# Performance work log

Hardware: AMD Instinct MI355X
Metric: run time of the kernel (lower is better)

Reference implementation:

```python
import jax, jax.numpy as jnp
import numpy as np


def setup_inputs() -> dict:
    key = jax.random.key(0)
    ks = jax.random.split(key, 5)
    B, S, D, F = 4, 2048, 1024, 4096
    scale_w1 = 1.0 / np.sqrt(D)
    scale_w2 = 1.0 / np.sqrt(F)
    return {
        "hidden_states": jax.random.normal(ks[0], (B, S, D), dtype=jnp.float32),
        "W1": jax.random.normal(ks[1], (F, D), dtype=jnp.float32) * scale_w1,
        "b1": jax.random.normal(ks[2], (F,), dtype=jnp.float32) * 0.02,
        "W2": jax.random.normal(ks[3], (D, F), dtype=jnp.float32) * scale_w2,
        "b2": jax.random.normal(ks[4], (D,), dtype=jnp.float32) * 0.02,
    }


def _sigmoid_poly(h):
    # cubic polynomial sigmoid approximation: 0.5 + 0.25*h - 0.0208*h^3
    h2 = h * h
    h3 = h2 * h
    return 0.5 + 0.25 * h + (-0.0208) * h3


def reference(hidden_states, W1, b1, W2, b2):
    # secure linear projection == plain affine: x @ W.T + b
    h = jnp.einsum("bsd,fd->bsf", hidden_states, W1) + b1  # [B,S,F]
    sw = h * _sigmoid_poly(h)                               # swish via poly sigmoid
    out = jnp.einsum("bsf,df->bsd", sw, W2) + b2            # [B,S,D]
    return out
```

## Files before the change

### kernel.cpp

```cpp
#include <hip/hip_runtime.h>
#include <hip/hip_bf16.h>

typedef __bf16 bf16_t;
typedef __bf16 bf16x8 __attribute__((ext_vector_type(8)));
typedef float f32x4 __attribute__((ext_vector_type(4)));

__global__ __launch_bounds__(256) void cast3_f32_to_bf16(
    const float* __restrict__ a, bf16_t* __restrict__ ao, int na8,
    const float* __restrict__ b, bf16_t* __restrict__ bo, int nb8,
    const float* __restrict__ c, bf16_t* __restrict__ co, int nc8) {
  int i = blockIdx.x * blockDim.x + threadIdx.x;
  const float* in;
  bf16_t* out;
  int j;
  if (i < na8) {
    in = a; out = ao; j = i;
  } else if (i < na8 + nb8) {
    in = b; out = bo; j = i - na8;
  } else if (i < na8 + nb8 + nc8) {
    in = c; out = co; j = i - na8 - nb8;
  } else {
    return;
  }
  const float4* in4 = (const float4*)in;
  float4 f0 = in4[2 * j];
  float4 f1 = in4[2 * j + 1];
  bf16x8 o;
  o[0] = (bf16_t)f0.x; o[1] = (bf16_t)f0.y;
  o[2] = (bf16_t)f0.z; o[3] = (bf16_t)f0.w;
  o[4] = (bf16_t)f1.x; o[5] = (bf16_t)f1.y;
  o[6] = (bf16_t)f1.z; o[7] = (bf16_t)f1.w;
  ((bf16x8*)out)[j] = o;
}

__device__ __forceinline__ void gload_lds16(const bf16_t* g, bf16_t* l) {
  __builtin_amdgcn_global_load_lds(
      (const __attribute__((address_space(1))) void*)g,
      (__attribute__((address_space(3))) void*)l,
      16, 0, 0);
}

template <bool SWISH>
__global__ __launch_bounds__(256) void gemm_bt(
    const bf16_t* __restrict__ A, const bf16_t* __restrict__ B,
    const float* __restrict__ bias, void* __restrict__ Cout,
    int M, int N, int K, int XW, int px, int py) {
  const int tid  = threadIdx.x;
  const int wave = tid >> 6;
  const int lane = tid & 63;

  const int bid = blockIdx.x;
  const int xcd = bid & 7;
  const int idx = bid >> 3;
  const int cx = xcd % XW;
  const int cy = xcd / XW;
  const int bx = cx * px + idx % px;
  const int by = cy * py + idx / px;
  const int tileM = by << 7;
  const int tileN = bx << 7;

  __shared__ __align__(16) bf16_t sA[128 * 64];
  __shared__ __align__(16) bf16_t sB[128 * 64];

  const int srow = (wave << 3) + (lane >> 3);
  const int gcol = (((lane & 7) ^ (lane >> 3)) << 3);
  const bf16_t* gA = A + (size_t)(tileM + srow) * K + gcol;
  const bf16_t* gB = B + (size_t)(tileN + srow) * K + gcol;
  bf16_t* lA = sA + (size_t)(wave << 3) * 64;
  bf16_t* lB = sB + (size_t)(wave << 3) * 64;

  const int wr = wave >> 1;
  const int wc = wave & 1;
  const int fRow = lane & 15;
  const int c0 = lane >> 4;
  const int swz = lane & 7;
  const int p0 = c0 ^ swz;
  const int d1 = (((p0 ^ 4) - p0) << 3);
  const bf16x8* pA[4];
  const bf16x8* pB[4];
#pragma unroll
  for (int i = 0; i < 4; ++i) {
    const int lrA = wr * 64 + i * 16 + fRow;
    const int lrB = wc * 64 + i * 16 + fRow;
    pA[i] = (const bf16x8*)(sA + lrA * 64 + p0 * 8);
    pB[i] = (const bf16x8*)(sB + lrB * 64 + p0 * 8);
  }

  f32x4 acc[4][4] = {};

  for (int kt = 0; kt < K; kt += 64) {
#pragma unroll
    for (int r = 0; r < 4; ++r) {
      gload_lds16(gA + kt + (size_t)(r * 32) * K, lA + r * 32 * 64);
      gload_lds16(gB + kt + (size_t)(r * 32) * K, lB + r * 32 * 64);
    }
    __syncthreads();

    bf16x8 a0[4], b0[4];
#pragma unroll
    for (int i = 0; i < 4; ++i) {
      a0[i] = *pA[i];
      b0[i] = *pB[i];
    }
#pragma unroll
    for (int i = 0; i < 4; ++i)
#pragma unroll
      for (int j = 0; j < 4; ++j)
        acc[i][j] = __builtin_amdgcn_mfma_f32_16x16x32_bf16(
            a0[i], b0[j], acc[i][j], 0, 0, 0);

    bf16x8 a1[4], b1[4];
#pragma unroll
    for (int i = 0; i < 4; ++i) {
      a1[i] = *(const bf16x8*)((const bf16_t*)pA[i] + d1);
      b1[i] = *(const bf16x8*)((const bf16_t*)pB[i] + d1);
    }
#pragma unroll
    for (int i = 0; i < 4; ++i)
#pragma unroll
      for (int j = 0; j < 4; ++j)
        acc[i][j] = __builtin_amdgcn_mfma_f32_16x16x32_bf16(
            a1[i], b1[j], acc[i][j], 0, 0, 0);
    __syncthreads();
  }

  const int cRow0 = tileM + wr * 64 + ((lane >> 4) << 2);
  const int cCol0 = tileN + wc * 64 + (lane & 15);
#pragma unroll
  for (int j = 0; j < 4; ++j) {
    const int col = cCol0 + j * 16;
    const float bv = bias[col];
#pragma unroll
    for (int i = 0; i < 4; ++i) {
      const int row = cRow0 + i * 16;
#pragma unroll
      for (int r = 0; r < 4; ++r) {
        float h = acc[i][j][r] + bv;
        if constexpr (SWISH) {
          float h3 = h * h * h;
          float sw = h * (0.5f + 0.25f * h - 0.0208f * h3);
          ((bf16_t*)Cout)[(size_t)(row + r) * N + col] = (bf16_t)sw;
        } else {
          ((float*)Cout)[(size_t)(row + r) * N + col] = h;
        }
      }
    }
  }
}

extern "C" void kernel_launch(void* const* d_in, const int* in_sizes, int n_in,
                              void* d_out, int out_size, void* d_ws,
                              size_t ws_size, hipStream_t stream) {
  const float* X  = (const float*)d_in[0];
  const float* W1 = (const float*)d_in[1];
  const float* b1 = (const float*)d_in[2];
  const float* W2 = (const float*)d_in[3];
  const float* b2 = (const float*)d_in[4];
  float* out = (float*)d_out;

  const int F = in_sizes[2];
  const int D = in_sizes[4];
  const int M = in_sizes[0] / D;

  bf16_t* Xb  = (bf16_t*)d_ws;
  bf16_t* W1b = Xb + (size_t)M * D;
  bf16_t* W2b = W1b + (size_t)F * D;
  bf16_t* SW  = W2b + (size_t)D * F;

  const int nX = (M * D) / 8, nW1 = (F * D) / 8, nW2 = (D * F) / 8;
  const int nTot = nX + nW1 + nW2;
  cast3_f32_to_bf16<<<(nTot + 255) / 256, 256, 0, stream>>>(
      X, Xb, nX, W1, W1b, nW1, W2, W2b, nW2);

  {
    const int gx = F / 128, gy = M / 128;
    const int XW = 2, XH = 4;
    const int px = gx / XW, py = gy / XH;
    gemm_bt<true><<<gx * gy, 256, 0, stream>>>(
        Xb, W1b, b1, (void*)SW, M, F, D, XW, px, py);
  }

  {
    const int gx = D / 128, gy = M / 128;
    const int XW = 1, XH = 8;
    const int px = gx / XW, py = gy / XH;
    gemm_bt<false><<<gx * gy, 256, 0, stream>>>(
        SW, W2b, b2, (void*)out, M, D, F, XW, px, py);
  }
}
```

Measured before the change: 266.0 us.

## Use 256x128 tiles with 32x32 MFMA and double-buffered LDS prefetch

Restructures the GEMM kernel to a 256x128 output tile per block, switching from 16x16x32 to 32x32x16 bf16 MFMA with f32x16 accumulators. It uses K-step 32 with a double-buffered LDS pipeline so the next tile's global-to-LDS loads overlap the current MFMAs, which needs only one barrier per iteration. Launch bounds now request 2 blocks per SM and the XCD grid mapping is retuned. The goal is more data reuse per LDS byte and hidden load latency. The cost is fewer blocks in the grid, especially for the second GEMM, which has only 8x32 blocks, and a different swizzle and output store pattern.

```diff
diff --git a/kernel.cpp b/kernel.cpp
--- a/kernel.cpp
+++ b/kernel.cpp
@@ -3,7 +3,7 @@
 
 typedef __bf16 bf16_t;
 typedef __bf16 bf16x8 __attribute__((ext_vector_type(8)));
-typedef float f32x4 __attribute__((ext_vector_type(4)));
+typedef float f32x16 __attribute__((ext_vector_type(16)));
 
 __global__ __launch_bounds__(256) void cast3_f32_to_bf16(
     const float* __restrict__ a, bf16_t* __restrict__ ao, int na8,
@@ -41,11 +41,11 @@
 }
 
 template <bool SWISH>
-__global__ __launch_bounds__(256) void gemm_bt(
+__global__ __launch_bounds__(256, 2) void gemm_bt(
     const bf16_t* __restrict__ A, const bf16_t* __restrict__ B,
     const float* __restrict__ bias, void* __restrict__ Cout,
     int M, int N, int K, int XW, int px, int py) {
-  const int tid  = threadIdx.x;
+  const int tid = threadIdx.x;
   const int wave = tid >> 6;
   const int lane = tid & 63;
 
@@ -56,92 +56,96 @@
   const int cy = xcd / XW;
   const int bx = cx * px + idx % px;
   const int by = cy * py + idx / px;
-  const int tileM = by << 7;
+  const int tileM = by << 8;
   const int tileN = bx << 7;
 
-  __shared__ __align__(16) bf16_t sA[128 * 64];
-  __shared__ __align__(16) bf16_t sB[128 * 64];
+  __shared__ __align__(16) bf16_t sA[2 * 256 * 32];
+  __shared__ __align__(16) bf16_t sB[2 * 128 * 32];
 
-  const int srow = (wave << 3) + (lane >> 3);
-  const int gcol = (((lane & 7) ^ (lane >> 3)) << 3);
-  const bf16_t* gA = A + (size_t)(tileM + srow) * K + gcol;
-  const bf16_t* gB = B + (size_t)(tileN + srow) * K + gcol;
-  bf16_t* lA = sA + (size_t)(wave << 3) * 64;
-  bf16_t* lB = sB + (size_t)(wave << 3) * 64;
+  const int lrow = lane >> 2;
+  const int clog = (lane & 3) ^ (lrow & 3);
+  const bf16_t* gA = A + (size_t)(tileM + wave * 64 + lrow) * K + clog * 8;
+  const bf16_t* gB = B + (size_t)(tileN + wave * 32 + lrow) * K + clog * 8;
+  bf16_t* lA = sA + (wave * 64) * 32;
+  bf16_t* lB = sB + (wave * 32) * 32;
 
-  const int wr = wave >> 1;
-  const int wc = wave & 1;
-  const int fRow = lane & 15;
-  const int c0 = lane >> 4;
-  const int swz = lane & 7;
-  const int p0 = c0 ^ swz;
-  const int d1 = (((p0 ^ 4) - p0) << 3);
-  const bf16x8* pA[4];
-  const bf16x8* pB[4];
+  const int wr = wave >> 1, wc = wave & 1;
+  const int cswz = (((lane >> 5) ^ (lane & 3)) << 3);
+  int offA[4], offB[2];
+#pragma unroll
+  for (int i = 0; i < 4; ++i)
+    offA[i] = (wr * 128 + i * 32 + (lane & 31)) * 32 + cswz;
+#pragma unroll
+  for (int j = 0; j < 2; ++j)
+    offB[j] = (wc * 64 + j * 32 + (lane & 31)) * 32 + cswz;
+
+  f32x16 acc[4][2] = {};
+
+  const int niter = K >> 5;
+
+#pragma unroll
+  for (int r = 0; r < 4; ++r)
+    gload_lds16(gA + (size_t)(r * 16) * K, lA + r * 16 * 32);
+#pragma unroll
+  for (int r = 0; r < 2; ++r)
+    gload_lds16(gB + (size_t)(r * 16) * K, lB + r * 16 * 32);
+
+  for (int it = 0; it < niter; ++it) {
+    __syncthreads();
+    const int p = it & 1;
+    if (it + 1 < niter) {
+      const int kt = (it + 1) << 5;
+      const int q = p ^ 1;
+#pragma unroll
+      for (int r = 0; r < 4; ++r)
+        gload_lds16(gA + kt + (size_t)(r * 16) * K,
+                    lA + q * (256 * 32) + r * 16 * 32);
+#pragma unroll
+      for (int r = 0; r < 2; ++r)
+        gload_lds16(gB + kt + (size_t)(r * 16) * K,
+                    lB + q * (128 * 32) + r * 16 * 32);
+    }
+    const bf16_t* bA = sA + p * (256 * 32);
+    const bf16_t* bB = sB + p * (128 * 32);
+    bf16x8 af[2][4], bg[2][2];
+#pragma unroll
+    for (int s = 0; s < 2; ++s) {
+      const int sx = s << 4;
+#pragma unroll
+      for (int i = 0; i < 4; ++i)
+        af[s][i] = *(const bf16x8*)(bA + (offA[i] ^ sx));
+#pragma unroll
+      for (int j = 0; j < 2; ++j)
+        bg[s][j] = *(const bf16x8*)(bB + (offB[j] ^ sx));
+    }
+#pragma unroll
+    for (int s = 0; s < 2; ++s)
+#pragma unroll
+      for (int i = 0; i < 4; ++i)
+#pragma unroll
+        for (int j = 0; j < 2; ++j)
+          acc[i][j] = __builtin_amdgcn_mfma_f32_32x32x16_bf16(
+              af[s][i], bg[s][j], acc[i][j], 0, 0, 0);
+  }
+
+  const int halfsel = (lane >> 5) << 2;
 #pragma unroll
   for (int i = 0; i < 4; ++i) {
-    const int lrA = wr * 64 + i * 16 + fRow;
-    const int lrB = wc * 64 + i * 16 + fRow;
-    pA[i] = (const bf16x8*)(sA + lrA * 64 + p0 * 8);
-    pB[i] = (const bf16x8*)(sB + lrB * 64 + p0 * 8);
-  }
-
-  f32x4 acc[4][4] = {};
-
-  for (int kt = 0; kt < K; kt += 64) {
+    const int row0 = tileM + wr * 128 + i * 32 + halfsel;
 #pragma unroll
-    for (int r = 0; r < 4; ++r) {
-      gload_lds16(gA + kt + (size_t)(r * 32) * K, lA + r * 32 * 64);
-      gload_lds16(gB + kt + (size_t)(r * 32) * K, lB + r * 32 * 64);
-    }
-    __syncthreads();
-
-    bf16x8 a0[4], b0[4];
+    for (int j = 0; j < 2; ++j) {
+      const int col = tileN + wc * 64 + j * 32 + (lane & 31);
+      const float bv = bias[col];
 #pragma unroll
-    for (int i = 0; i < 4; ++i) {
-      a0[i] = *pA[i];
-      b0[i] = *pB[i];
-    }
-#pragma unroll
-    for (int i = 0; i < 4; ++i)
-#pragma unroll
-      for (int j = 0; j < 4; ++j)
-        acc[i][j] = __builtin_amdgcn_mfma_f32_16x16x32_bf16(
-            a0[i], b0[j], acc[i][j], 0, 0, 0);
-
-    bf16x8 a1[4], b1[4];
-#pragma unroll
-    for (int i = 0; i < 4; ++i) {
-      a1[i] = *(const bf16x8*)((const bf16_t*)pA[i] + d1);
-      b1[i] = *(const bf16x8*)((const bf16_t*)pB[i] + d1);
-    }
-#pragma unroll
-    for (int i = 0; i < 4; ++i)
-#pragma unroll
-      for (int j = 0; j < 4; ++j)
-        acc[i][j] = __builtin_amdgcn_mfma_f32_16x16x32_bf16(
-            a1[i], b1[j], acc[i][j], 0, 0, 0);
-    __syncthreads();
-  }
-
-  const int cRow0 = tileM + wr * 64 + ((lane >> 4) << 2);
-  const int cCol0 = tileN + wc * 64 + (lane & 15);
-#pragma unroll
-  for (int j = 0; j < 4; ++j) {
-    const int col = cCol0 + j * 16;
-    const float bv = bias[col];
-#pragma unroll
-    for (int i = 0; i < 4; ++i) {
-      const int row = cRow0 + i * 16;
-#pragma unroll
-      for (int r = 0; r < 4; ++r) {
+      for (int r = 0; r < 16; ++r) {
+        const int row = row0 + (r & 3) + ((r >> 2) << 3);
         float h = acc[i][j][r] + bv;
         if constexpr (SWISH) {
           float h3 = h * h * h;
           float sw = h * (0.5f + 0.25f * h - 0.0208f * h3);
-          ((bf16_t*)Cout)[(size_t)(row + r) * N + col] = (bf16_t)sw;
+          ((bf16_t*)Cout)[(size_t)row * N + col] = (bf16_t)sw;
         } else {
-          ((float*)Cout)[(size_t)(row + r) * N + col] = h;
+          ((float*)Cout)[(size_t)row * N + col] = h;
         }
       }
     }
@@ -173,16 +177,16 @@
       X, Xb, nX, W1, W1b, nW1, W2, W2b, nW2);
 
   {
-    const int gx = F / 128, gy = M / 128;
-    const int XW = 2, XH = 4;
+    const int gx = F / 128, gy = M / 256;
+    const int XW = 4, XH = 2;
     const int px = gx / XW, py = gy / XH;
     gemm_bt<true><<<gx * gy, 256, 0, stream>>>(
         Xb, W1b, b1, (void*)SW, M, F, D, XW, px, py);
   }
 
   {
-    const int gx = D / 128, gy = M / 128;
-    const int XW = 1, XH = 8;
+    const int gx = D / 128, gy = M / 256;
+    const int XW = 8, XH = 1;
     const int px = gx / XW, py = gy / XH;
     gemm_bt<false><<<gx * gy, 256, 0, stream>>>(
         SW, W2b, b2, (void*)out, M, D, F, XW, px, py);
```

Measured after the change: 337.4 us. 26.9% more time.
